# Kernel optimization log

Hardware: AMD Instinct MI355X
Metric: run time of the kernel (lower is better)

## Reference

```python
import jax, jax.numpy as jnp
import numpy as np

# Directable[TL_table[i]] for i = 0..7: (dx, dy) with dx=horizontal shift, dy=vertical shift
# dx=+1 -> shift right (zero-fill col 0), dx=-1 -> shift left; dy=+1 -> shift down, dy=-1 -> shift up.
DIRS = [(1, 1), (0, 1), (-1, 1), (1, 0), (-1, 0), (1, -1), (0, -1), (-1, -1)]


def _shift(img, dx, dy):
    # img: [B, H, W]; zero-padded shift equivalent to bmm with the sparse translation matrices
    if dx == 1:
        img = jnp.pad(img[..., :-1], ((0, 0), (0, 0), (1, 0)))
    elif dx == -1:
        img = jnp.pad(img[..., 1:], ((0, 0), (0, 0), (0, 1)))
    if dy == 1:
        img = jnp.pad(img[:, :-1, :], ((0, 0), (1, 0), (0, 0)))
    elif dy == -1:
        img = jnp.pad(img[:, 1:, :], ((0, 0), (0, 1), (0, 0)))
    return img


def _bce(p, t):
    # torch F.binary_cross_entropy clamps log terms at -100
    logp = jnp.maximum(jnp.log(p), -100.0)
    log1mp = jnp.maximum(jnp.log(1.0 - p), -100.0)
    return -jnp.mean(t * logp + (1.0 - t) * log1mp)


def setup_inputs() -> dict:
    key = jax.random.key(0)
    k1, k2, k3 = jax.random.split(key, 3)
    B, C, H, W = 16, 8, 512, 512
    c_map = jax.random.normal(k1, (B, C, H, W), dtype=jnp.float32)
    target = jax.random.randint(k2, (B, 1, H, W), 0, 2, dtype=jnp.int32)
    con_target = jax.random.randint(k3, (B, C, H, W), 0, 2, dtype=jnp.int32)
    return {"c_map": c_map, "target": target, "con_target": con_target}


def reference(c_map, target, con_target):
    target = target.astype(jnp.float32)        # [B,1,H,W]
    con_target = con_target.astype(jnp.float32)  # [B,8,H,W]

    p = jax.nn.sigmoid(c_map)  # [B,8,H,W]

    # Bilateral voting: shifted[i] = shift(p[:, 7-i]) in direction DIRS[i]
    shifted = jnp.stack(
        [_shift(p[:, 7 - i], dx, dy) for i, (dx, dy) in enumerate(DIRS)], axis=1
    )  # [B,8,H,W]
    vote_out = p * shifted                       # [B,8,H,W] (== bimap.squeeze(1))
    final_pred = jnp.max(vote_out, axis=1, keepdims=True)  # [B,1,H,W]

    # dice loss (sums over dims (1,2) of the 4D tensors, as in the original)
    smooth = 0.001
    i_sum = jnp.sum(target, axis=(1, 2))
    j_sum = jnp.sum(final_pred, axis=(1, 2))
    inter = jnp.sum(target * final_pred, axis=(1, 2))
    loss_dice = jnp.mean(1.0 - (2.0 * inter + smooth) / (i_sum + j_sum + smooth))

    # edge (decouple) loss
    sum_conn = jnp.sum(con_target, axis=1)  # [B,H,W]
    edge = ((sum_conn < 8) & (sum_conn > 0)).astype(p.dtype)
    pred_min = jnp.min(vote_out, axis=1) * edge
    decouple_loss = _bce(pred_min, jnp.zeros_like(pred_min))

    bce_loss = _bce(final_pred, target)
    conmap_l = _bce(p, con_target)
    bimap_l = _bce(vote_out, con_target)

    return 0.8 * conmap_l + decouple_loss + 0.2 * bimap_l + bce_loss + loss_dice
```

## Files before the change

### kernel.cpp

```cpp
#include <hip/hip_runtime.h>

namespace {
constexpr int Bn = 16, Hn = 512, Wn = 512;
constexpr int HW  = Hn * Wn;
constexpr int CHW = 8 * HW;
constexpr int NCOL = Bn * Wn;
constexpr int WALK = 2;
constexpr int GX   = Hn / (2 * WALK);
constexpr int NBLK = GX * Bn;
constexpr int FBLK = 32;

constexpr float L2E  = 1.4426950408889634f;
constexpr float LN2  = 0.6931471805599453f;
constexpr float CLMP = -144.26950408889634f;

__device__ __forceinline__ float frcp(float x) { return __builtin_amdgcn_rcpf(x); }
#if __has_builtin(__builtin_amdgcn_exp2f)
__device__ __forceinline__ float fexp2(float x) { return __builtin_amdgcn_exp2f(x); }
#else
__device__ __forceinline__ float fexp2(float x) { return exp2f(x); }
#endif
#if __has_builtin(__builtin_amdgcn_logf)
__device__ __forceinline__ float flog2(float x) { return __builtin_amdgcn_logf(x); }
#else
__device__ __forceinline__ float flog2(float x) { return log2f(x); }
#endif
}


__global__ __launch_bounds__(256) void bicon_main(
    const float* __restrict__ c_map,
    const int*   __restrict__ target,
    const int*   __restrict__ con_target,
    float* __restrict__ col_i, float* __restrict__ col_j, float* __restrict__ col_x,
    double* __restrict__ bscal)
{
    const int tid  = threadIdx.x;
    const int lane = tid & 63;
    const int wv   = tid >> 6;
    const int half = wv & 1;
    const int rg   = wv >> 1;
    const int b    = blockIdx.y;
    const int hstart = blockIdx.x * (2 * WALK) + rg * WALK;
    const int wq   = half * 256 + lane * 4;

    const float* cm = c_map      + (size_t)b * CHW;
    const int*   ct = con_target + (size_t)b * CHW;
    const int*   tg = target     + (size_t)b * HW;

    float s_con = 0.f, s_bi = 0.f, s_bce = 0.f, s_dec = 0.f;
    float ci[4] = {0, 0, 0, 0}, cj[4] = {0, 0, 0, 0}, cx[4] = {0, 0, 0, 0};

    auto sig4 = [&](const float4& v, float s[4]) {
        s[0] = frcp(1.f + fexp2(-v.x * L2E));
        s[1] = frcp(1.f + fexp2(-v.y * L2E));
        s[2] = frcp(1.f + fexp2(-v.z * L2E));
        s[3] = frcp(1.f + fexp2(-v.w * L2E));
    };

    float C0[4], C1[4], C2[4], P5[4], P6[4], P7[4];
    {
        const int pb = hstart * Wn + wq;
        sig4(*(const float4*)(cm + 0 * HW + pb), C0);
        sig4(*(const float4*)(cm + 1 * HW + pb), C1);
        sig4(*(const float4*)(cm + 2 * HW + pb), C2);
    }
    if (hstart > 0) {
        const int pb = (hstart - 1) * Wn + wq;
        sig4(*(const float4*)(cm + 5 * HW + pb), P5);
        sig4(*(const float4*)(cm + 6 * HW + pb), P6);
        sig4(*(const float4*)(cm + 7 * HW + pb), P7);
    } else {
#pragma unroll
        for (int k = 0; k < 4; ++k) { P5[k] = 0.f; P6[k] = 0.f; P7[k] = 0.f; }
    }

    const bool edR = (wq + 4 == Wn);
    const bool edL = (wq == 0);

    int h = hstart;
#pragma unroll 1
    for (int r = 0; r < WALK; ++r, ++h) {
        const int  base  = h * Wn + wq;
        const bool hasDn = (h + 1 < Hn);
        const bool hasUp = (h > 0);

        const float4 xa3 = *(const float4*)(cm + 3 * HW + base);
        const float4 xa4 = *(const float4*)(cm + 4 * HW + base);
        const float4 xa5 = *(const float4*)(cm + 5 * HW + base);
        const float4 xa6 = *(const float4*)(cm + 6 * HW + base);
        const float4 xa7 = *(const float4*)(cm + 7 * HW + base);
        const float4 xf0 = *(const float4*)(cm + 0 * HW + base + Wn);
        const float4 xf1 = *(const float4*)(cm + 1 * HW + base + Wn);
        const float4 xf2 = *(const float4*)(cm + 2 * HW + base + Wn);
        const float bx0 = cm[0 * HW + base + Wn + 4];
        const float bx2 = cm[2 * HW + base + Wn - 1];
        const float bx3 = cm[3 * HW + base + 4];
        const float bx4 = cm[4 * HW + base - 1];
        const float bx5 = cm[5 * HW + base - Wn + 4];
        const float bx7 = cm[7 * HW + base - Wn - 1];
        const int4  t4  = *(const int4*)(tg + base);

        unsigned lo = 0u;
#pragma unroll
        for (int c = 0; c < 8; ++c) {
            const int4 u = *(const int4*)(ct + c * HW + base);
            lo |= ((unsigned)u.x << c)        | ((unsigned)u.y << (8 + c)) |
                  ((unsigned)u.z << (16 + c)) | ((unsigned)u.w << (24 + c));
        }

        float dp[4] = {1.f, 1.f, 1.f, 1.f};
        float ys[4] = {0.f, 0.f, 0.f, 0.f};
        float c3[4], c4[4], c5[4], c6[4], c7[4];
        auto fresh = [&](int c, const float4& v, float s[4]) {
            const float xs[4] = {v.x, v.y, v.z, v.w};
#pragma unroll
            for (int k = 0; k < 4; ++k) {
                const float y = xs[k] * L2E;
                const float e = fexp2(-y);
                const float d = 1.f + e;
                s[k] = frcp(d);
                dp[k] *= d;
                ys[k] += ((lo >> (8 * k + c)) & 1u) ? 0.f : y;
            }
        };
        fresh(3, xa3, c3); fresh(4, xa4, c4); fresh(5, xa5, c5);
        fresh(6, xa6, c6); fresh(7, xa7, c7);

#pragma unroll
        for (int k = 0; k < 4; ++k) {
            const float q0 = ((lo >> (8 * k + 0)) & 1u) ? C0[k] : 1.f - C0[k];
            const float q1 = ((lo >> (8 * k + 1)) & 1u) ? C1[k] : 1.f - C1[k];
            const float q2 = ((lo >> (8 * k + 2)) & 1u) ? C2[k] : 1.f - C2[k];
            s_con += flog2(q0 * q1 * q2) - flog2(dp[k]) - ys[k];
        }

        float F0[4], F1[4], F2[4];
        sig4(xf0, F0); sig4(xf1, F1); sig4(xf2, F2);
        const float s0b = frcp(1.f + fexp2(-bx0 * L2E));
        const float s2b = frcp(1.f + fexp2(-bx2 * L2E));
        const float s3b = frcp(1.f + fexp2(-bx3 * L2E));
        const float s4b = frcp(1.f + fexp2(-bx4 * L2E));
        const float s5b = frcp(1.f + fexp2(-bx5 * L2E));
        const float s7b = frcp(1.f + fexp2(-bx7 * L2E));

        float n0[4], n1[4], n2[4], n3[4], n4[4], n5[4], n6[4], n7[4];
#pragma unroll
        for (int k = 0; k < 3; ++k) {
            n0[k] = F0[k + 1]; n3[k] = c3[k + 1]; n5[k] = P5[k + 1];
            n2[k + 1] = F2[k]; n4[k + 1] = c4[k]; n7[k + 1] = P7[k];
        }
        n0[3] = edR ? 0.f : s0b;  n3[3] = edR ? 0.f : s3b;  n5[3] = edR ? 0.f : s5b;
        n2[0] = edL ? 0.f : s2b;  n4[0] = edL ? 0.f : s4b;  n7[0] = edL ? 0.f : s7b;
#pragma unroll
        for (int k = 0; k < 4; ++k) {
            n1[k] = hasDn ? F1[k] : 0.f;
            n6[k] = hasUp ? P6[k] : 0.f;
            if (!hasDn) { n0[k] = 0.f; n2[k] = 0.f; }
            if (!hasUp) { n5[k] = 0.f; n7[k] = 0.f; }
        }

        float vmax[4] = {0.f, 0.f, 0.f, 0.f}, vmin[4] = {2.f, 2.f, 2.f, 2.f};
        float pr[4]   = {1.f, 1.f, 1.f, 1.f};
        float zc[4]   = {0.f, 0.f, 0.f, 0.f};
        auto vote = [&](int i, const float p[4], const float n[4]) {
#pragma unroll
            for (int k = 0; k < 4; ++k) {
                const float v = p[k] * n[k];
                vmax[k] = fmaxf(vmax[k], v);
                vmin[k] = fminf(vmin[k], v);
                const bool bit = (lo >> (8 * k + i)) & 1u;
                const bool z   = bit && (v == 0.f);
                float sel = bit ? v : 1.f - v;
                sel = z ? 1.f : sel;
                zc[k] += z ? 1.f : 0.f;
                pr[k] *= sel;
            }
        };
        vote(0, C0, n7); vote(1, C1, n6); vote(2, C2, n5); vote(3, c3, n4);
#pragma unroll
        for (int k = 0; k < 4; ++k) { s_bi += flog2(pr[k]); pr[k] = 1.f; }
        vote(4, c4, n3); vote(5, c5, n2); vote(6, c6, n1); vote(7, c7, n0);
#pragma unroll
        for (int k = 0; k < 4; ++k) { s_bi += flog2(pr[k]) + CLMP * zc[k]; }

        const int tk[4] = {t4.x, t4.y, t4.z, t4.w};
#pragma unroll
        for (int k = 0; k < 4; ++k) {
            const float fm = vmax[k];
            s_bce += fmaxf(flog2(tk[k] ? fm : 1.f - fm), CLMP);
            const int sc = __popc((int)((lo >> (8 * k)) & 0xffu));
            s_dec += (sc > 0 && sc < 8) ? fmaxf(flog2(1.f - vmin[k]), CLMP) : 0.f;
            ci[k] += (float)tk[k];
            cj[k] += fm;
            cx[k] += tk[k] ? fm : 0.f;
        }

#pragma unroll
        for (int k = 0; k < 4; ++k) {
            C0[k] = F0[k]; C1[k] = F1[k]; C2[k] = F2[k];
            P5[k] = c5[k]; P6[k] = c6[k]; P7[k] = c7[k];
        }
    }

    __shared__ float cred[3][4][256];
#pragma unroll
    for (int k = 0; k < 4; ++k) {
        cred[0][wv][(lane << 2) + k] = ci[k];
        cred[1][wv][(lane << 2) + k] = cj[k];
        cred[2][wv][(lane << 2) + k] = cx[k];
    }

#pragma unroll
    for (int off = 32; off > 0; off >>= 1) {
        s_con += __shfl_down(s_con, off);
        s_bi  += __shfl_down(s_bi,  off);
        s_bce += __shfl_down(s_bce, off);
        s_dec += __shfl_down(s_dec, off);
    }
    __shared__ float wred[4][4];
    if (lane == 0) {
        wred[wv][0] = s_con * LN2; wred[wv][1] = s_bi * LN2;
        wred[wv][2] = s_bce * LN2; wred[wv][3] = s_dec * LN2;
    }
    __syncthreads();

#pragma unroll
    for (int j = tid; j < 512; j += 256) {
        const int hj = j >> 8, cidx = j & 255;
        atomicAdd(&col_i[b * Wn + j], cred[0][hj][cidx] + cred[0][hj + 2][cidx]);
        atomicAdd(&col_j[b * Wn + j], cred[1][hj][cidx] + cred[1][hj + 2][cidx]);
        atomicAdd(&col_x[b * Wn + j], cred[2][hj][cidx] + cred[2][hj + 2][cidx]);
    }
    if (tid < 4) {
        bscal[((size_t)blockIdx.y * GX + blockIdx.x) * 4 + tid] =
            (double)(wred[0][tid] + wred[1][tid] + wred[2][tid] + wred[3][tid]);
    }
}

__global__ __launch_bounds__(256) void bicon_finish(
    const float* __restrict__ col_i,
    const float* __restrict__ col_j,
    const float* __restrict__ col_x,
    const double* __restrict__ bscal,
    float* __restrict__ out)
{
    const int tid = threadIdx.x;
    const int col = blockIdx.x * 256 + tid;

    double part;
    {
        const float fi = col_i[col], fj = col_j[col], fx = col_x[col];
        part = (1.0 - (2.0 * (double)fx + 0.001) /
                      ((double)fi + (double)fj + 0.001)) / 8192.0;
    }
    if (tid < 64) {
        const int s = blockIdx.x * 64 + tid;
        const double c0 = bscal[s * 4 + 0], c1 = bscal[s * 4 + 1];
        const double c2 = bscal[s * 4 + 2], c3 = bscal[s * 4 + 3];
        part += -0.8 * c0 / 33554432.0 - 0.2 * c1 / 33554432.0
                - c2 / 4194304.0 - c3 / 4194304.0;
    }
#pragma unroll
    for (int off = 32; off > 0; off >>= 1) part += __shfl_down(part, off);
    __shared__ double red[4];
    if ((tid & 63) == 0) red[tid >> 6] = part;
    __syncthreads();
    if (tid == 0) atomicAdd(out, (float)(red[0] + red[1] + red[2] + red[3]));
}

extern "C" void kernel_launch(void* const* d_in, const int* in_sizes, int n_in,
                              void* d_out, int out_size, void* d_ws, size_t ws_size,
                              hipStream_t stream) {
    const float* c_map      = (const float*)d_in[0];
    const int*   target     = (const int*)d_in[1];
    const int*   con_target = (const int*)d_in[2];
    float* out = (float*)d_out;

    char* ws = (char*)d_ws;
    float*  col_i = (float*)ws;
    float*  col_j = col_i + NCOL;
    float*  col_x = col_j + NCOL;
    double* bscal = (double*)(ws + 3 * NCOL * sizeof(float));

    hipMemsetAsync(d_ws, 0, 3 * NCOL * sizeof(float), stream);
    hipMemsetAsync(d_out, 0, sizeof(float), stream);

    dim3 grid(GX, Bn);
    dim3 block(256);
    bicon_main<<<grid, block, 0, stream>>>(c_map, target, con_target,
                                           col_i, col_j, col_x, bscal);
    bicon_finish<<<FBLK, 256, 0, stream>>>(col_i, col_j, col_x, bscal, out);
}
```

Measured before the change: 303.1 us.

## Give each thread two columns over four rows and drop shared column reduction

```diff
diff --git a/kernel.cpp b/kernel.cpp
--- a/kernel.cpp
+++ b/kernel.cpp
@@ -5,8 +5,8 @@
 constexpr int HW  = Hn * Wn;
 constexpr int CHW = 8 * HW;
 constexpr int NCOL = Bn * Wn;
-constexpr int WALK = 2;
-constexpr int GX   = Hn / (2 * WALK);
+constexpr int WALK = 4;
+constexpr int GX   = Hn / WALK;
 constexpr int NBLK = GX * Bn;
 constexpr int FBLK = 32;
 
@@ -38,44 +38,40 @@
     const int tid  = threadIdx.x;
     const int lane = tid & 63;
     const int wv   = tid >> 6;
-    const int half = wv & 1;
-    const int rg   = wv >> 1;
     const int b    = blockIdx.y;
-    const int hstart = blockIdx.x * (2 * WALK) + rg * WALK;
-    const int wq   = half * 256 + lane * 4;
+    const int hstart = blockIdx.x * WALK;
+    const int wq   = wv * 128 + lane * 2;
 
     const float* cm = c_map      + (size_t)b * CHW;
     const int*   ct = con_target + (size_t)b * CHW;
     const int*   tg = target     + (size_t)b * HW;
 
     float s_con = 0.f, s_bi = 0.f, s_bce = 0.f, s_dec = 0.f;
-    float ci[4] = {0, 0, 0, 0}, cj[4] = {0, 0, 0, 0}, cx[4] = {0, 0, 0, 0};
-
-    auto sig4 = [&](const float4& v, float s[4]) {
+    float ci[2] = {0, 0}, cj[2] = {0, 0}, cx[2] = {0, 0};
+
+    auto sig2 = [&](const float2& v, float s[2]) {
         s[0] = frcp(1.f + fexp2(-v.x * L2E));
         s[1] = frcp(1.f + fexp2(-v.y * L2E));
-        s[2] = frcp(1.f + fexp2(-v.z * L2E));
-        s[3] = frcp(1.f + fexp2(-v.w * L2E));
     };
 
-    float C0[4], C1[4], C2[4], P5[4], P6[4], P7[4];
+    float C0[2], C1[2], C2[2], P5[2], P6[2], P7[2];
     {
         const int pb = hstart * Wn + wq;
-        sig4(*(const float4*)(cm + 0 * HW + pb), C0);
-        sig4(*(const float4*)(cm + 1 * HW + pb), C1);
-        sig4(*(const float4*)(cm + 2 * HW + pb), C2);
+        sig2(*(const float2*)(cm + 0 * HW + pb), C0);
+        sig2(*(const float2*)(cm + 1 * HW + pb), C1);
+        sig2(*(const float2*)(cm + 2 * HW + pb), C2);
     }
     if (hstart > 0) {
         const int pb = (hstart - 1) * Wn + wq;
-        sig4(*(const float4*)(cm + 5 * HW + pb), P5);
-        sig4(*(const float4*)(cm + 6 * HW + pb), P6);
-        sig4(*(const float4*)(cm + 7 * HW + pb), P7);
+        sig2(*(const float2*)(cm + 5 * HW + pb), P5);
+        sig2(*(const float2*)(cm + 6 * HW + pb), P6);
+        sig2(*(const float2*)(cm + 7 * HW + pb), P7);
     } else {
 #pragma unroll
-        for (int k = 0; k < 4; ++k) { P5[k] = 0.f; P6[k] = 0.f; P7[k] = 0.f; }
-    }
-
-    const bool edR = (wq + 4 == Wn);
+        for (int k = 0; k < 2; ++k) { P5[k] = 0.f; P6[k] = 0.f; P7[k] = 0.f; }
+    }
+
+    const bool edR = (wq + 2 == Wn);
     const bool edL = (wq == 0);
 
     int h = hstart;
@@ -85,37 +81,36 @@
         const bool hasDn = (h + 1 < Hn);
         const bool hasUp = (h > 0);
 
-        const float4 xa3 = *(const float4*)(cm + 3 * HW + base);
-        const float4 xa4 = *(const float4*)(cm + 4 * HW + base);
-        const float4 xa5 = *(const float4*)(cm + 5 * HW + base);
-        const float4 xa6 = *(const float4*)(cm + 6 * HW + base);
-        const float4 xa7 = *(const float4*)(cm + 7 * HW + base);
-        const float4 xf0 = *(const float4*)(cm + 0 * HW + base + Wn);
-        const float4 xf1 = *(const float4*)(cm + 1 * HW + base + Wn);
-        const float4 xf2 = *(const float4*)(cm + 2 * HW + base + Wn);
-        const float bx0 = cm[0 * HW + base + Wn + 4];
+        const float2 xa3 = *(const float2*)(cm + 3 * HW + base);
+        const float2 xa4 = *(const float2*)(cm + 4 * HW + base);
+        const float2 xa5 = *(const float2*)(cm + 5 * HW + base);
+        const float2 xa6 = *(const float2*)(cm + 6 * HW + base);
+        const float2 xa7 = *(const float2*)(cm + 7 * HW + base);
+        const float2 xf0 = *(const float2*)(cm + 0 * HW + base + Wn);
+        const float2 xf1 = *(const float2*)(cm + 1 * HW + base + Wn);
+        const float2 xf2 = *(const float2*)(cm + 2 * HW + base + Wn);
+        const float bx0 = cm[0 * HW + base + Wn + 2];
         const float bx2 = cm[2 * HW + base + Wn - 1];
-        const float bx3 = cm[3 * HW + base + 4];
+        const float bx3 = cm[3 * HW + base + 2];
         const float bx4 = cm[4 * HW + base - 1];
-        const float bx5 = cm[5 * HW + base - Wn + 4];
+        const float bx5 = cm[5 * HW + base - Wn + 2];
         const float bx7 = cm[7 * HW + base - Wn - 1];
-        const int4  t4  = *(const int4*)(tg + base);
+        const int2  t2  = *(const int2*)(tg + base);
 
         unsigned lo = 0u;
 #pragma unroll
         for (int c = 0; c < 8; ++c) {
-            const int4 u = *(const int4*)(ct + c * HW + base);
-            lo |= ((unsigned)u.x << c)        | ((unsigned)u.y << (8 + c)) |
-                  ((unsigned)u.z << (16 + c)) | ((unsigned)u.w << (24 + c));
-        }
-
-        float dp[4] = {1.f, 1.f, 1.f, 1.f};
-        float ys[4] = {0.f, 0.f, 0.f, 0.f};
-        float c3[4], c4[4], c5[4], c6[4], c7[4];
-        auto fresh = [&](int c, const float4& v, float s[4]) {
-            const float xs[4] = {v.x, v.y, v.z, v.w};
-#pragma unroll
-            for (int k = 0; k < 4; ++k) {
+            const int2 u = *(const int2*)(ct + c * HW + base);
+            lo |= ((unsigned)u.x << c) | ((unsigned)u.y << (8 + c));
+        }
+
+        float dp[2] = {1.f, 1.f};
+        float ys[2] = {0.f, 0.f};
+        float c3[2], c4[2], c5[2], c6[2], c7[2];
+        auto fresh = [&](int c, const float2& v, float s[2]) {
+            const float xs[2] = {v.x, v.y};
+#pragma unroll
+            for (int k = 0; k < 2; ++k) {
                 const float y = xs[k] * L2E;
                 const float e = fexp2(-y);
                 const float d = 1.f + e;
@@ -128,15 +123,15 @@
         fresh(6, xa6, c6); fresh(7, xa7, c7);
 
 #pragma unroll
-        for (int k = 0; k < 4; ++k) {
+        for (int k = 0; k < 2; ++k) {
             const float q0 = ((lo >> (8 * k + 0)) & 1u) ? C0[k] : 1.f - C0[k];
             const float q1 = ((lo >> (8 * k + 1)) & 1u) ? C1[k] : 1.f - C1[k];
             const float q2 = ((lo >> (8 * k + 2)) & 1u) ? C2[k] : 1.f - C2[k];
-            s_con += flog2(q0 * q1 * q2) - flog2(dp[k]) - ys[k];
-        }
-
-        float F0[4], F1[4], F2[4];
-        sig4(xf0, F0); sig4(xf1, F1); sig4(xf2, F2);
+            s_con += flog2(q0 * q1 * q2 * frcp(dp[k])) - ys[k];
+        }
+
+        float F0[2], F1[2], F2[2];
+        sig2(xf0, F0); sig2(xf1, F1); sig2(xf2, F2);
         const float s0b = frcp(1.f + fexp2(-bx0 * L2E));
         const float s2b = frcp(1.f + fexp2(-bx2 * L2E));
         const float s3b = frcp(1.f + fexp2(-bx3 * L2E));
@@ -144,28 +139,25 @@
         const float s5b = frcp(1.f + fexp2(-bx5 * L2E));
         const float s7b = frcp(1.f + fexp2(-bx7 * L2E));
 
-        float n0[4], n1[4], n2[4], n3[4], n4[4], n5[4], n6[4], n7[4];
-#pragma unroll
-        for (int k = 0; k < 3; ++k) {
-            n0[k] = F0[k + 1]; n3[k] = c3[k + 1]; n5[k] = P5[k + 1];
-            n2[k + 1] = F2[k]; n4[k + 1] = c4[k]; n7[k + 1] = P7[k];
-        }
-        n0[3] = edR ? 0.f : s0b;  n3[3] = edR ? 0.f : s3b;  n5[3] = edR ? 0.f : s5b;
+        float n0[2], n1[2], n2[2], n3[2], n4[2], n5[2], n6[2], n7[2];
+        n0[0] = F0[1];  n3[0] = c3[1];  n5[0] = P5[1];
+        n2[1] = F2[0];  n4[1] = c4[0];  n7[1] = P7[0];
+        n0[1] = edR ? 0.f : s0b;  n3[1] = edR ? 0.f : s3b;  n5[1] = edR ? 0.f : s5b;
         n2[0] = edL ? 0.f : s2b;  n4[0] = edL ? 0.f : s4b;  n7[0] = edL ? 0.f : s7b;
 #pragma unroll
-        for (int k = 0; k < 4; ++k) {
+        for (int k = 0; k < 2; ++k) {
             n1[k] = hasDn ? F1[k] : 0.f;
             n6[k] = hasUp ? P6[k] : 0.f;
             if (!hasDn) { n0[k] = 0.f; n2[k] = 0.f; }
             if (!hasUp) { n5[k] = 0.f; n7[k] = 0.f; }
         }
 
-        float vmax[4] = {0.f, 0.f, 0.f, 0.f}, vmin[4] = {2.f, 2.f, 2.f, 2.f};
-        float pr[4]   = {1.f, 1.f, 1.f, 1.f};
-        float zc[4]   = {0.f, 0.f, 0.f, 0.f};
-        auto vote = [&](int i, const float p[4], const float n[4]) {
-#pragma unroll
-            for (int k = 0; k < 4; ++k) {
+        float vmax[2] = {0.f, 0.f}, vmin[2] = {2.f, 2.f};
+        float pr[2]   = {1.f, 1.f};
+        float zc[2]   = {0.f, 0.f};
+        auto vote = [&](int i, const float p[2], const float n[2]) {
+#pragma unroll
+            for (int k = 0; k < 2; ++k) {
                 const float v = p[k] * n[k];
                 vmax[k] = fmaxf(vmax[k], v);
                 vmin[k] = fminf(vmin[k], v);
@@ -178,15 +170,13 @@
             }
         };
         vote(0, C0, n7); vote(1, C1, n6); vote(2, C2, n5); vote(3, c3, n4);
-#pragma unroll
-        for (int k = 0; k < 4; ++k) { s_bi += flog2(pr[k]); pr[k] = 1.f; }
         vote(4, c4, n3); vote(5, c5, n2); vote(6, c6, n1); vote(7, c7, n0);
 #pragma unroll
-        for (int k = 0; k < 4; ++k) { s_bi += flog2(pr[k]) + CLMP * zc[k]; }
-
-        const int tk[4] = {t4.x, t4.y, t4.z, t4.w};
-#pragma unroll
-        for (int k = 0; k < 4; ++k) {
+        for (int k = 0; k < 2; ++k) { s_bi += flog2(pr[k]) + CLMP * zc[k]; }
+
+        const int tk[2] = {t2.x, t2.y};
+#pragma unroll
+        for (int k = 0; k < 2; ++k) {
             const float fm = vmax[k];
             s_bce += fmaxf(flog2(tk[k] ? fm : 1.f - fm), CLMP);
             const int sc = __popc((int)((lo >> (8 * k)) & 0xffu));
@@ -197,18 +187,20 @@
         }
 
 #pragma unroll
-        for (int k = 0; k < 4; ++k) {
+        for (int k = 0; k < 2; ++k) {
             C0[k] = F0[k]; C1[k] = F1[k]; C2[k] = F2[k];
             P5[k] = c5[k]; P6[k] = c6[k]; P7[k] = c7[k];
         }
     }
 
-    __shared__ float cred[3][4][256];
-#pragma unroll
-    for (int k = 0; k < 4; ++k) {
-        cred[0][wv][(lane << 2) + k] = ci[k];
-        cred[1][wv][(lane << 2) + k] = cj[k];
-        cred[2][wv][(lane << 2) + k] = cx[k];
+    {
+        const int col = b * Wn + wq;
+        atomicAdd(&col_i[col],     ci[0]);
+        atomicAdd(&col_i[col + 1], ci[1]);
+        atomicAdd(&col_j[col],     cj[0]);
+        atomicAdd(&col_j[col + 1], cj[1]);
+        atomicAdd(&col_x[col],     cx[0]);
+        atomicAdd(&col_x[col + 1], cx[1]);
     }
 
 #pragma unroll
@@ -224,14 +216,6 @@
         wred[wv][2] = s_bce * LN2; wred[wv][3] = s_dec * LN2;
     }
     __syncthreads();
-
-#pragma unroll
-    for (int j = tid; j < 512; j += 256) {
-        const int hj = j >> 8, cidx = j & 255;
-        atomicAdd(&col_i[b * Wn + j], cred[0][hj][cidx] + cred[0][hj + 2][cidx]);
-        atomicAdd(&col_j[b * Wn + j], cred[1][hj][cidx] + cred[1][hj + 2][cidx]);
-        atomicAdd(&col_x[b * Wn + j], cred[2][hj][cidx] + cred[2][hj + 2][cidx]);
-    }
     if (tid < 4) {
         bscal[((size_t)blockIdx.y * GX + blockIdx.x) * 4 + tid] =
             (double)(wred[0][tid] + wred[1][tid] + wred[2][tid] + wred[3][tid]);
```

Measured after the change: 312.6 us. 3.1% more time.
